# Kernel tuning notes

Measured on AMD Instinct MI355X. Metric: run time of the kernel, lower is better.

## Reference

```python
import jax, jax.numpy as jnp
import numpy as np

N = 100_000   # nodes
E = 1_600_000 # edges (avg degree 16)
D = 64        # in_dim == hidden_dim


def setup_inputs() -> dict:
    key = jax.random.key(0)
    ks = jax.random.split(key, 9)
    scale = 1.0 / np.sqrt(D)
    x = jax.random.normal(ks[0], (N, D), jnp.float32)
    edge_index = jax.random.randint(ks[1], (2, E), 0, N, dtype=jnp.int32)
    W0 = jax.random.normal(ks[2], (D, D), jnp.float32) * scale
    b0 = jnp.zeros((D,), jnp.float32)
    W1 = jax.random.normal(ks[3], (D, D), jnp.float32) * scale
    b1 = jnp.zeros((D,), jnp.float32)
    W2 = jax.random.normal(ks[4], (D, D), jnp.float32) * scale
    b2 = jnp.zeros((D,), jnp.float32)
    return {"x": x, "edge_index": edge_index, "W0": W0, "b0": b0,
            "W1": W1, "b1": b1, "W2": W2, "b2": b2}


def _gcn_layer(h, W, b, src, dst, norm):
    # h: [N, D]; src/dst: [E+N] (self-loops included); norm: [E+N]
    h = h @ W                                  # dense transform [N, D]
    msg = h[src] * norm[:, None]               # gather + scale  [E+N, D]
    out = jax.ops.segment_sum(msg, dst, num_segments=N)  # scatter-add [N, D]
    return out + b


def reference(x, edge_index, W0, b0, W1, b1, W2, b2):
    loops = jnp.arange(N, dtype=edge_index.dtype)
    src = jnp.concatenate([edge_index[0], loops])  # [E+N]
    dst = jnp.concatenate([edge_index[1], loops])  # [E+N]
    # symmetric GCN normalization with self-loops (PyG gcn_norm)
    deg = jax.ops.segment_sum(jnp.ones_like(dst, dtype=x.dtype), dst, num_segments=N)
    d_inv = jnp.where(deg > 0, jax.lax.rsqrt(deg), 0.0)
    norm = d_inv[src] * d_inv[dst]                 # [E+N]
    for W, b in ((W0, b0), (W1, b1), (W2, b2)):
        x = jax.nn.relu(_gcn_layer(x, W, b, src, dst, norm))
    return x
```

## Files before the change

### kernel.cpp

```cpp
#include <hip/hip_runtime.h>
#include <hip/hip_fp16.h>


#define THREADS 256
#define BSH     9
#define BNODES  512
#define BCAP    9216
#define BPAD    16
#define CHUNK   4096

#if defined(__has_builtin)
#if __has_builtin(__builtin_amdgcn_fdot2) && __has_builtin(__builtin_amdgcn_perm)
#define USE_DOT2 1
#endif
#endif

typedef __attribute__((ext_vector_type(2))) _Float16 h2v;
typedef __attribute__((ext_vector_type(8))) _Float16 f16x8;
typedef __attribute__((ext_vector_type(4))) float    f32x4;

__global__ __launch_bounds__(THREADS)
void zero_kernel(int* __restrict__ p, int n) {
    int i = blockIdx.x * blockDim.x + threadIdx.x;
    if (i < n) p[i] = 0;
}

__global__ __launch_bounds__(THREADS)
void bin_kernel(const int* __restrict__ src, const int* __restrict__ dst,
                int* __restrict__ bcur, int* __restrict__ sbuf, int E) {
    __shared__ int cntb[THREADS];
    __shared__ int lstart[THREADS];
    __shared__ int gbase[THREADS];
    __shared__ int lcur[THREADS];
    __shared__ int tmp[THREADS];
    __shared__ int stagep[CHUNK];
    __shared__ unsigned char stageb[CHUNK];
    int tid = threadIdx.x;
    int e0  = blockIdx.x * CHUNK;
    int cnt = min(CHUNK, E - e0);
    int dreg[16];
#pragma unroll
    for (int j = 0; j < 16; ++j) {
        int i = tid + j * THREADS;
        dreg[j] = (i < cnt) ? dst[e0 + i] : -1;
    }
    cntb[tid] = 0;
    __syncthreads();
#pragma unroll
    for (int j = 0; j < 16; ++j)
        if (dreg[j] >= 0) atomicAdd(&cntb[dreg[j] >> BSH], 1);
    __syncthreads();
    int v = cntb[tid];
    tmp[tid] = v;
    __syncthreads();
    for (int off = 1; off < THREADS; off <<= 1) {
        int t = (tid >= off) ? tmp[tid - off] : 0;
        __syncthreads();
        tmp[tid] += t;
        __syncthreads();
    }
    lstart[tid] = tmp[tid] - v;
    lcur[tid]   = 0;
    if (v > 0) gbase[tid] = atomicAdd(&bcur[tid * BPAD], v);
    __syncthreads();
#pragma unroll
    for (int j = 0; j < 16; ++j) {
        int i = tid + j * THREADS;
        if (i < cnt) {
            int s = src[e0 + i];
            int d = dreg[j];
            int b = d >> BSH;
            int pos = atomicAdd(&lcur[b], 1);
            int idx = lstart[b] + pos;
            stagep[idx] = (s << BSH) | (d & (BNODES - 1));
            stageb[idx] = (unsigned char)b;
        }
    }
    __syncthreads();
    for (int i = tid; i < cnt; i += THREADS) {
        int b = stageb[i];
        sbuf[(size_t)b * BCAP + gbase[b] + (i - lstart[b])] = stagep[i];
    }
}

__global__ __launch_bounds__(THREADS)
void bscan_kernel(const int* __restrict__ bcur, int* __restrict__ bbase,
                  int NB, int* __restrict__ rowptr, int N, int E) {
    __shared__ int tmp[THREADS];
    int tid = threadIdx.x;
    int c = (tid < NB) ? min(bcur[tid * BPAD], BCAP) : 0;
    tmp[tid] = c;
    __syncthreads();
    for (int off = 1; off < THREADS; off <<= 1) {
        int t = (tid >= off) ? tmp[tid - off] : 0;
        __syncthreads();
        tmp[tid] += t;
        __syncthreads();
    }
    if (tid < NB) bbase[tid] = tmp[tid] - c;
    if (tid == 0) rowptr[N] = E;
}

__global__ __launch_bounds__(THREADS)
void finalize_kernel(const int* __restrict__ sbuf, const int* __restrict__ bcur,
                     const int* __restrict__ bbase, int* __restrict__ rowptr,
                     float* __restrict__ dinv, int* __restrict__ csrc, int N) {
    __shared__ int lcnt[BNODES];
    __shared__ int lexcl[BNODES];
    __shared__ int lcur[BNODES];
    __shared__ int tmp[THREADS];
    int b   = blockIdx.x;
    int tid = threadIdx.x;
    int cnt = min(bcur[b * BPAD], BCAP);
    int gb  = bbase[b];
    const int* sb = sbuf + (size_t)b * BCAP;
    for (int i = tid; i < BNODES; i += THREADS) { lcnt[i] = 0; lcur[i] = 0; }
    __syncthreads();
    for (int e = tid; e < cnt; e += THREADS)
        atomicAdd(&lcnt[sb[e] & (BNODES - 1)], 1);
    __syncthreads();
    int a0 = lcnt[2 * tid], a1 = lcnt[2 * tid + 1];
    int s  = a0 + a1;
    tmp[tid] = s;
    __syncthreads();
    for (int off = 1; off < THREADS; off <<= 1) {
        int t = (tid >= off) ? tmp[tid - off] : 0;
        __syncthreads();
        tmp[tid] += t;
        __syncthreads();
    }
    int ex = tmp[tid] - s;
    lexcl[2 * tid]     = ex;
    lexcl[2 * tid + 1] = ex + a0;
    int node = (b << BSH) + 2 * tid;
    if (node < N) {
        rowptr[node] = gb + ex;
        dinv[node]   = rsqrtf((float)(a0 + 1));
    }
    if (node + 1 < N) {
        rowptr[node + 1] = gb + ex + a0;
        dinv[node + 1]   = rsqrtf((float)(a1 + 1));
    }
    __syncthreads();
    for (int e = tid; e < cnt; e += THREADS) {
        int vv  = sb[e];
        int d   = vv & (BNODES - 1);
        int pos = atomicAdd(&lcur[d], 1);
        csrc[gb + lexcl[d] + pos] = vv >> BSH;
    }
}

template <typename IT>
__global__ __launch_bounds__(THREADS)
void gemm64_kernel(const IT* __restrict__ X, __half* __restrict__ H,
                   const float* __restrict__ W, const float* __restrict__ dinv,
                   int n) {
    int lane = threadIdx.x & 63;
    int qk   = lane >> 4;
    int l16  = lane & 15;
    f16x8 bf[4][2];
#pragma unroll
    for (int t = 0; t < 4; ++t)
#pragma unroll
        for (int h = 0; h < 2; ++h) {
            const float* wp = W + (size_t)(32 * h + qk * 8) * 64 + 16 * t + l16;
#pragma unroll
            for (int j = 0; j < 8; ++j)
                bf[t][h][j] = (_Float16)wp[j * 64];
        }
    int wave  = (blockIdx.x * blockDim.x + threadIdx.x) >> 6;
    int nw    = (gridDim.x * blockDim.x) >> 6;
    int ntile = (n + 15) >> 4;
    for (int tile = wave; tile < ntile; tile += nw) {
        int rbase = tile << 4;
        int arow  = rbase + l16;
        if (arow >= n) arow = n - 1;
        f16x8 A0, A1;
        if constexpr (sizeof(IT) == 4) {
            const float4* xp = (const float4*)((const float*)X + (size_t)arow * 64 + qk * 8);
            float4 a0 = xp[0], a1 = xp[1];
            float4 a2 = xp[8], a3 = xp[9];
            A0[0] = (_Float16)a0.x; A0[1] = (_Float16)a0.y;
            A0[2] = (_Float16)a0.z; A0[3] = (_Float16)a0.w;
            A0[4] = (_Float16)a1.x; A0[5] = (_Float16)a1.y;
            A0[6] = (_Float16)a1.z; A0[7] = (_Float16)a1.w;
            A1[0] = (_Float16)a2.x; A1[1] = (_Float16)a2.y;
            A1[2] = (_Float16)a2.z; A1[3] = (_Float16)a2.w;
            A1[4] = (_Float16)a3.x; A1[5] = (_Float16)a3.y;
            A1[6] = (_Float16)a3.z; A1[7] = (_Float16)a3.w;
        } else {
            const int4* xp = (const int4*)((const __half*)X + (size_t)arow * 64 + qk * 8);
            A0 = __builtin_bit_cast(f16x8, xp[0]);
            A1 = __builtin_bit_cast(f16x8, xp[4]);
        }
        f32x4 acc[4];
#pragma unroll
        for (int t = 0; t < 4; ++t) {
            acc[t] = (f32x4){0.f, 0.f, 0.f, 0.f};
            acc[t] = __builtin_amdgcn_mfma_f32_16x16x32_f16(bf[t][0], A0, acc[t], 0, 0, 0);
            acc[t] = __builtin_amdgcn_mfma_f32_16x16x32_f16(bf[t][1], A1, acc[t], 0, 0, 0);
        }
        int row = rbase + l16;
        if (row < n) {
            float dv = dinv[row];
            __half* hp = H + (size_t)row * 64 + qk * 4;
#pragma unroll
            for (int t = 0; t < 4; ++t) {
                __half2 p0 = __floats2half2_rn(acc[t][0] * dv, acc[t][1] * dv);
                __half2 p1 = __floats2half2_rn(acc[t][2] * dv, acc[t][3] * dv);
                int2 pv;
                pv.x = *(const int*)&p0;
                pv.y = *(const int*)&p1;
                *(int2*)(hp + 16 * t) = pv;
            }
        }
    }
}

__device__ __forceinline__ void pairdot(const int4& hA, const int4& hB,
                                        bool vA, bool vB, float* accf) {
#ifdef USE_DOT2
    unsigned mb = (vA ? 0x3C00u : 0u) | (vB ? 0x3C000000u : 0u);
    h2v m2 = __builtin_bit_cast(h2v, mb);
    const unsigned* pa = (const unsigned*)&hA;
    const unsigned* pb = (const unsigned*)&hB;
#pragma unroll
    for (int j = 0; j < 4; ++j) {
        unsigned p0 = __builtin_amdgcn_perm(pb[j], pa[j], 0x05040100);
        unsigned p1 = __builtin_amdgcn_perm(pb[j], pa[j], 0x07060302);
        accf[2 * j]     = __builtin_amdgcn_fdot2(
            __builtin_bit_cast(h2v, p0), m2, accf[2 * j], false);
        accf[2 * j + 1] = __builtin_amdgcn_fdot2(
            __builtin_bit_cast(h2v, p1), m2, accf[2 * j + 1], false);
    }
#else
    float mA = vA ? 1.f : 0.f, mB = vB ? 1.f : 0.f;
    const __half2* ha = (const __half2*)&hA;
    const __half2* hb = (const __half2*)&hB;
#pragma unroll
    for (int j = 0; j < 4; ++j) {
        float2 fa = __half22float2(ha[j]);
        float2 fb = __half22float2(hb[j]);
        accf[2 * j]     = fmaf(fa.x, mA, accf[2 * j]);
        accf[2 * j]     = fmaf(fb.x, mB, accf[2 * j]);
        accf[2 * j + 1] = fmaf(fa.y, mA, accf[2 * j + 1]);
        accf[2 * j + 1] = fmaf(fb.y, mB, accf[2 * j + 1]);
    }
#endif
}

template <typename OT>
__global__ __launch_bounds__(THREADS)
void agg_kernel(const __half* __restrict__ H, OT* __restrict__ Y,
                const int* __restrict__ rowptr, const int* __restrict__ csrc,
                const float* __restrict__ dinv, const float* __restrict__ bias,
                int n) {
    int lane = threadIdx.x & 63;
    int half = lane >> 5;
    int hl   = lane & 31;
    int grp  = hl >> 3;
    int sub  = lane & 7;
    int fl   = sub * 8;
    const int4* H4 = (const int4*)H;
    int wave = (blockIdx.x * blockDim.x + threadIdx.x) >> 6;
    int nw   = (gridDim.x * blockDim.x) >> 6;
    int np   = (n + 1) >> 1;
    float4 bv0 = *(const float4*)(bias + fl);
    float4 bv1 = *(const float4*)(bias + fl + 4);
    int wp = wave;
    if (wp >= np) return;
    int node = min(2 * wp + half, n - 1);
    int k0 = rowptr[node], k1 = rowptr[node + 1];
    while (true) {
        int wpn = wp + nw;
        int noden = 0, k0n = 0, k1n = 0;
        bool more = wpn < np;
        if (more) {
            noden = min(2 * wpn + half, n - 1);
            k0n = rowptr[noden];
            k1n = rowptr[noden + 1];
        }
        float accf[8] = {0.f, 0.f, 0.f, 0.f, 0.f, 0.f, 0.f, 0.f};
        if (grp == 0) {
            int4 hv = H4[(size_t)node * 8 + sub];
            const __half2* hh = (const __half2*)&hv;
#pragma unroll
            for (int j = 0; j < 4; ++j) {
                float2 f = __half22float2(hh[j]);
                accf[2 * j]     += f.x;
                accf[2 * j + 1] += f.y;
            }
        }
        for (int basek = k0; basek < k1; basek += 16) {
            int  kk0 = basek + grp;
            int  kk1 = kk0 + 4, kk2 = kk0 + 8, kk3 = kk0 + 12;
            bool v0 = kk0 < k1, v1 = kk1 < k1, v2 = kk2 < k1, v3 = kk3 < k1;
            int  s0 = v0 ? csrc[kk0] : 0;
            int  s1 = v1 ? csrc[kk1] : 0;
            int  s2 = v2 ? csrc[kk2] : 0;
            int  s3 = v3 ? csrc[kk3] : 0;
            int4 h0 = H4[(size_t)s0 * 8 + sub];
            int4 h1 = H4[(size_t)s1 * 8 + sub];
            int4 h2 = H4[(size_t)s2 * 8 + sub];
            int4 h3 = H4[(size_t)s3 * 8 + sub];
            pairdot(h0, h1, v0, v1, accf);
            pairdot(h2, h3, v2, v3, accf);
        }
#pragma unroll
        for (int j = 0; j < 8; ++j) {
            float a = accf[j];
            a += __shfl_xor(a, 8);
            a += __shfl_xor(a, 16);
            accf[j] = a;
        }
        if (grp == 0 && 2 * wp + half < n) {
            float di = dinv[node];
            float o[8];
            o[0] = fmaxf(fmaf(accf[0], di, bv0.x), 0.f);
            o[1] = fmaxf(fmaf(accf[1], di, bv0.y), 0.f);
            o[2] = fmaxf(fmaf(accf[2], di, bv0.z), 0.f);
            o[3] = fmaxf(fmaf(accf[3], di, bv0.w), 0.f);
            o[4] = fmaxf(fmaf(accf[4], di, bv1.x), 0.f);
            o[5] = fmaxf(fmaf(accf[5], di, bv1.y), 0.f);
            o[6] = fmaxf(fmaf(accf[6], di, bv1.z), 0.f);
            o[7] = fmaxf(fmaf(accf[7], di, bv1.w), 0.f);
            if constexpr (sizeof(OT) == 2) {
                __half2 hh[4];
#pragma unroll
                for (int j = 0; j < 4; ++j)
                    hh[j] = __floats2half2_rn(o[2 * j], o[2 * j + 1]);
                *(int4*)((__half*)Y + (size_t)node * 64 + fl) =
                    *(const int4*)hh;
            } else {
                float4 o0 = make_float4(o[0], o[1], o[2], o[3]);
                float4 o1 = make_float4(o[4], o[5], o[6], o[7]);
                *(float4*)((float*)Y + (size_t)node * 64 + fl)     = o0;
                *(float4*)((float*)Y + (size_t)node * 64 + fl + 4) = o1;
            }
        }
        if (!more) break;
        wp = wpn; node = noden; k0 = k0n; k1 = k1n;
    }
}

extern "C" void kernel_launch(void* const* d_in, const int* in_sizes, int n_in,
                              void* d_out, int out_size, void* d_ws, size_t ws_size,
                              hipStream_t stream) {
    const float* x  = (const float*)d_in[0];
    const int*   ei = (const int*)d_in[1];
    const float* W0 = (const float*)d_in[2];
    const float* b0 = (const float*)d_in[3];
    const float* W1 = (const float*)d_in[4];
    const float* b1 = (const float*)d_in[5];
    const float* W2 = (const float*)d_in[6];
    const float* b2 = (const float*)d_in[7];

    const int N = in_sizes[0] / 64;
    const int E = in_sizes[1] / 2;
    const int* src = ei;
    const int* dst = ei + E;
    const int NB = (N + BNODES - 1) >> BSH;

    char*  ws  = (char*)d_ws;
    size_t off = 0;
    auto alloc = [&](size_t bytes) -> void* {
        void* p = ws + off;
        off += (bytes + 255) & ~(size_t)255;
        return p;
    };
    int*    rowptr = (int*)   alloc((size_t)(N + 1) * 4);
    float*  dinv   = (float*) alloc((size_t)N * 4);
    int*    csrc   = (int*)   alloc((size_t)E * 4);
    int*    bcur   = (int*)   alloc((size_t)NB * BPAD * 4);
    int*    bbase  = (int*)   alloc((size_t)NB * 4);
    int*    sbuf   = (int*)   alloc((size_t)NB * BCAP * 4);
    __half* hbuf   = (__half*)alloc((size_t)N * 64 * 2);
    __half* act16  = (__half*)alloc((size_t)N * 64 * 2);
    float*  outb   = (float*)d_out;

    const int ngrid = 2048;
    const int ggrid = 782;
    const int bgrid = (E + CHUNK - 1) / CHUNK;
    const int zn    = NB * BPAD;

    zero_kernel    <<<(zn + THREADS - 1) / THREADS, THREADS, 0, stream>>>(bcur, zn);
    bin_kernel     <<<bgrid, THREADS, 0, stream>>>(src, dst, bcur, sbuf, E);
    bscan_kernel   <<<1,     THREADS, 0, stream>>>(bcur, bbase, NB, rowptr, N, E);
    finalize_kernel<<<NB,    THREADS, 0, stream>>>(sbuf, bcur, bbase, rowptr,
                                                   dinv, csrc, N);

    gemm64_kernel<float> <<<ggrid, THREADS, 0, stream>>>(x, hbuf, W0, dinv, N);
    agg_kernel<__half>   <<<ngrid, THREADS, 0, stream>>>(hbuf, act16, rowptr, csrc, dinv, b0, N);
    gemm64_kernel<__half><<<ggrid, THREADS, 0, stream>>>(act16, hbuf, W1, dinv, N);
    agg_kernel<__half>   <<<ngrid, THREADS, 0, stream>>>(hbuf, act16, rowptr, csrc, dinv, b1, N);
    gemm64_kernel<__half><<<ggrid, THREADS, 0, stream>>>(act16, hbuf, W2, dinv, N);
    agg_kernel<float>    <<<ngrid, THREADS, 0, stream>>>(hbuf, outb, rowptr, csrc, dinv, b2, N);
}
```

Before: 188.3 us.

## Split aggregation feature columns across block pairs and retune gemm grid

The aggregation kernel now splits each node's 64 features into two 32-feature halves handled by different blocks, chosen by a block-index bit. Each lane reads a quarter of a half-row, and 8 edge groups cover two edges per iteration instead of four. The aim is to spread the gathered bytes per wave over more edges, giving more memory-level parallelism and a better L2 access pattern, at the cost of reading the index and rowptr arrays twice and one extra shuffle stage. The gemm grid size is also raised.

Measured after the change: 253.5 us. 1.35x slower.

```diff
diff --git a/kernel.cpp b/kernel.cpp
--- a/kernel.cpp
+++ b/kernel.cpp
@@ -255,15 +255,20 @@
                 const int* __restrict__ rowptr, const int* __restrict__ csrc,
                 const float* __restrict__ dinv, const float* __restrict__ bias,
                 int n) {
+    int bid  = blockIdx.x;
+    int f    = (bid >> 2) & 1;
+    int lb   = (bid >> 3) * 4 + (bid & 3);
+    int nlb  = (int)gridDim.x >> 1;
     int lane = threadIdx.x & 63;
     int half = lane >> 5;
     int hl   = lane & 31;
-    int grp  = hl >> 3;
-    int sub  = lane & 7;
-    int fl   = sub * 8;
+    int grp  = hl >> 2;
+    int sub  = lane & 3;
+    int fl   = f * 32 + sub * 8;
+    int hoff = f * 4 + sub;
     const int4* H4 = (const int4*)H;
-    int wave = (blockIdx.x * blockDim.x + threadIdx.x) >> 6;
-    int nw   = (gridDim.x * blockDim.x) >> 6;
+    int wave = lb * (THREADS >> 6) + ((int)threadIdx.x >> 6);
+    int nw   = nlb * (THREADS >> 6);
     int np   = (n + 1) >> 1;
     float4 bv0 = *(const float4*)(bias + fl);
     float4 bv1 = *(const float4*)(bias + fl + 4);
@@ -282,33 +287,29 @@
         }
         float accf[8] = {0.f, 0.f, 0.f, 0.f, 0.f, 0.f, 0.f, 0.f};
         if (grp == 0) {
-            int4 hv = H4[(size_t)node * 8 + sub];
+            int4 hv = H4[(size_t)node * 8 + hoff];
             const __half2* hh = (const __half2*)&hv;
 #pragma unroll
             for (int j = 0; j < 4; ++j) {
-                float2 f = __half22float2(hh[j]);
-                accf[2 * j]     += f.x;
-                accf[2 * j + 1] += f.y;
+                float2 fe = __half22float2(hh[j]);
+                accf[2 * j]     += fe.x;
+                accf[2 * j + 1] += fe.y;
             }
         }
         for (int basek = k0; basek < k1; basek += 16) {
             int  kk0 = basek + grp;
-            int  kk1 = kk0 + 4, kk2 = kk0 + 8, kk3 = kk0 + 12;
-            bool v0 = kk0 < k1, v1 = kk1 < k1, v2 = kk2 < k1, v3 = kk3 < k1;
+            int  kk1 = kk0 + 8;
+            bool v0 = kk0 < k1, v1 = kk1 < k1;
             int  s0 = v0 ? csrc[kk0] : 0;
             int  s1 = v1 ? csrc[kk1] : 0;
-            int  s2 = v2 ? csrc[kk2] : 0;
-            int  s3 = v3 ? csrc[kk3] : 0;
-            int4 h0 = H4[(size_t)s0 * 8 + sub];
-            int4 h1 = H4[(size_t)s1 * 8 + sub];
-            int4 h2 = H4[(size_t)s2 * 8 + sub];
-            int4 h3 = H4[(size_t)s3 * 8 + sub];
+            int4 h0 = H4[(size_t)s0 * 8 + hoff];
+            int4 h1 = H4[(size_t)s1 * 8 + hoff];
             pairdot(h0, h1, v0, v1, accf);
-            pairdot(h2, h3, v2, v3, accf);
         }
 #pragma unroll
         for (int j = 0; j < 8; ++j) {
             float a = accf[j];
+            a += __shfl_xor(a, 4);
             a += __shfl_xor(a, 8);
             a += __shfl_xor(a, 16);
             accf[j] = a;
@@ -379,7 +380,7 @@
     float*  outb   = (float*)d_out;
 
     const int ngrid = 2048;
-    const int ggrid = 782;
+    const int ggrid = 1024;
     const int bgrid = (E + CHUNK - 1) / CHUNK;
     const int zn    = NB * BPAD;
 
```
